# Kernel optimization log

Measured on AMD Instinct MI355X. Metric: run time of the kernel, lower is better.

The kernel has to match this reference:

```python
import jax, jax.numpy as jnp
import numpy as np

NUM_HEADS = 8
FOCUSING_FACTOR = 3
EPS = 1e-6


def _focus(x, f):
    # focusing: x**f, renormalized to keep the original L2 norm per token
    n = jnp.linalg.norm(x, axis=-1, keepdims=True)
    xp = x ** f
    return xp / jnp.linalg.norm(xp, axis=-1, keepdims=True) * n


def _split_heads(x, h):
    # b n (h c) -> (b h) n c
    b, n, C = x.shape
    return x.reshape(b, n, h, C // h).transpose(0, 2, 1, 3).reshape(b * h, n, C // h)


def setup_inputs() -> dict:
    key = jax.random.key(0)
    ks = jax.random.split(key, 9)
    B, Nq, Nkv, C = 8, 4096, 4096, 512
    query = jax.random.normal(ks[0], (B, Nq, C), jnp.float32)
    key_in = jax.random.normal(ks[1], (B, Nkv, C), jnp.float32)
    value = jax.random.normal(ks[2], (B, Nkv, C), jnp.float32)
    Wq = jax.random.normal(ks[3], (C, C), jnp.float32) * 0.02
    Wk = jax.random.normal(ks[4], (C, C), jnp.float32) * 0.02
    Wv = jax.random.normal(ks[5], (C, C), jnp.float32) * 0.02
    Wp = jax.random.normal(ks[6], (C, C), jnp.float32) * 0.02
    bp = jnp.zeros((C,), jnp.float32)
    scale = jax.random.normal(ks[7], (1, 1, C), jnp.float32) * 0.02
    return {"query": query, "key_in": key_in, "value": value,
            "Wq": Wq, "Wk": Wk, "Wv": Wv, "Wp": Wp, "bp": bp,
            "scale": scale, "H": 64, "W": 64}


def reference(query, key_in, value, Wq, Wk, Wv, Wp, bp, scale, H, W):
    B, N, C = query.shape
    h = NUM_HEADS
    # projections (qkv_bias=False)
    q = jax.nn.relu(query @ Wq) + EPS
    k = jax.nn.relu(key_in @ Wk) + EPS
    v = value @ Wv
    s = jax.nn.softplus(scale)  # [1,1,C]
    q = q / s
    k = k / s
    q = _focus(q, FOCUSING_FACTOR)
    k = _focus(k, FOCUSING_FACTOR)
    q = _split_heads(q, h)  # [(B h), N, c]
    k = _split_heads(k, h)
    v = _split_heads(v, h)
    # z-normalizer: 1 / (q . sum_j k_j)
    z = 1.0 / (jnp.einsum('bic,bc->bi', q, k.sum(axis=1)) + EPS)
    # O(n) kv-aggregation path (i*j*(c+d) > c*d*(i+j) for these shapes)
    kv = jnp.einsum('bjc,bjd->bcd', k, v)
    x = jnp.einsum('bic,bcd,bi->bid', q, kv, z)
    # (b h) n c -> b n (h c)
    x = x.reshape(B, h, N, C // h).transpose(0, 2, 1, 3).reshape(B, N, C)
    # note: dwc(v) feature_map in the original is dead code (never added to x)
    return x @ Wp + bp
```

## Files before the change

kernel.cpp:

```cpp
#include <hip/hip_runtime.h>
#include <hip/hip_bf16.h>
#include <math.h>

typedef __attribute__((ext_vector_type(8))) short short8;
typedef __attribute__((ext_vector_type(4))) float f32x4;

#define MFMA16x16x32(A,B,C) __builtin_amdgcn_mfma_f32_16x16x32_bf16((A),(B),(C),0,0,0)

__device__ __forceinline__ short f2b(float x) {
  __hip_bfloat16 h = __float2bfloat16(x);
  short s; __builtin_memcpy(&s, &h, 2); return s;
}
__device__ __forceinline__ float b2f(short s) {
  __hip_bfloat16 h; __builtin_memcpy(&h, &s, 2); return __bfloat162float(h);
}

__global__ __launch_bounds__(256)
void prep_kernel(const float* __restrict__ Wq, const float* __restrict__ Wk,
                 const float* __restrict__ Wv, const float* __restrict__ Wp,
                 const float* __restrict__ scale,
                 short* __restrict__ wpack, float* __restrict__ spls)
{
  const int b = blockIdx.x;
  const int t = threadIdx.x;
  if (b == 64) {
    for (int i = t; i < 512; i += 256) {
      float x = scale[i];
      spls[i] = (x > 20.f) ? x : log1pf(expf(x));
    }
    return;
  }
  const float* Ws[4] = {Wq, Wk, Wv, Wp};
  const int w = b >> 4, kf16 = b & 15;
  const float* W = Ws[w];
  short* dst = wpack + (size_t)w * (512 * 512);
  __shared__ short lds[32 * 512];
  for (int i = 0; i < 64; ++i) {
    int idx = i * 256 + t;
    int r = idx >> 9, c = idx & 511;
    lds[idx] = f2b(W[(size_t)(kf16 * 32 + r) * 512 + c]);
  }
  __syncthreads();
  for (int s = 0; s < 8; ++s) {
    int slot = s * 256 + t;
    int nf = slot >> 6, l = slot & 63;
    int n = nf * 16 + (l & 15);
    int k0 = 8 * (l >> 4);
    short8 v;
#pragma unroll
    for (int jj = 0; jj < 8; ++jj) v[jj] = lds[(k0 + jj) * 512 + n];
    *(short8*)(dst + ((size_t)(kf16 * 32 + nf) * 64 + l) * 8) = v;
  }
}

__global__ __launch_bounds__(512, 2)
void proj_kernel(const float* __restrict__ Aq, const float* __restrict__ Ak,
                 const float* __restrict__ Av, const short* __restrict__ Ax,
                 const short* __restrict__ wpack, const float* __restrict__ spls,
                 short* __restrict__ qf, short* __restrict__ kpk,
                 short* __restrict__ vpk, const float* __restrict__ bp,
                 float* __restrict__ outf, int mode_base)
{
  __shared__ char smem[65536];
  __shared__ float pnorm[2][8][64];
  __shared__ float facs[64];
  short* tile = (short*)smem;
  const int t = threadIdx.x;
  const int lane = t & 63;
  const int wid = t >> 6;
  const int g = lane >> 4;
  const int cl = lane & 15;
  const int bid = blockIdx.x;
  const int mode = (mode_base == 3) ? 3 : (bid >> 9);
  const int rb = (bid & 511) << 6;
  const int sr = t >> 3;
  const int sc = t & 7;
  const int r1 = bid & 3;
  const int r2 = (bid >> 2) & 3;

  const float* Af = (mode == 0) ? Aq : (mode == 1) ? Ak : Av;
  const short8* wp8 = (const short8*)(wpack + (size_t)mode * (512 * 512));

  {
    char* dst = smem + sr * 272 + sc * 32;
    if (mode < 3) {
      const float* src = Af + (size_t)(rb + sr) * 512 + r1 * 128 + sc * 16;
      f32x4 a0 = *(const f32x4*)(src);
      f32x4 a1 = *(const f32x4*)(src + 4);
      f32x4 a2 = *(const f32x4*)(src + 8);
      f32x4 a3 = *(const f32x4*)(src + 12);
      short8 v0, v1;
#pragma unroll
      for (int j = 0; j < 4; ++j) {
        v0[j] = f2b(a0[j]); v0[4 + j] = f2b(a1[j]);
        v1[j] = f2b(a2[j]); v1[4 + j] = f2b(a3[j]);
      }
      *(short8*)dst = v0; *(short8*)(dst + 16) = v1;
    } else {
      const short* src = Ax + (size_t)(rb + sr) * 512 + r1 * 128 + sc * 16;
      *(short8*)dst = *(const short8*)src;
      *(short8*)(dst + 16) = *(const short8*)(src + 8);
    }
  }
  f32x4 zero4 = {0.f, 0.f, 0.f, 0.f};
  f32x4 acc[4][4];
#pragma unroll
  for (int rf = 0; rf < 4; ++rf)
#pragma unroll
    for (int cf = 0; cf < 4; ++cf) acc[rf][cf] = zero4;

  short8 bcur[4], bnxt[4];
  {
    const int kf0 = r1 * 4 + r2;
#pragma unroll
    for (int cf = 0; cf < 4; ++cf)
      bcur[cf] = wp8[((size_t)(kf0 * 32 + wid * 4 + cf)) * 64 + lane];
  }
  __syncthreads();

#pragma unroll
  for (int sl = 0; sl < 4; ++sl) {
    const int s_phys = (sl + r1) & 3;
    const int s_next = (s_phys + 1) & 3;
    char* cur = smem + (sl & 1) * 17408;
    f32x4 rA0, rA1, rA2, rA3;
    short8 rB0, rB1;
    if (sl < 3) {
      if (mode < 3) {
        const float* src = Af + (size_t)(rb + sr) * 512 + s_next * 128 + sc * 16;
        rA0 = *(const f32x4*)(src);
        rA1 = *(const f32x4*)(src + 4);
        rA2 = *(const f32x4*)(src + 8);
        rA3 = *(const f32x4*)(src + 12);
      } else {
        const short* src = Ax + (size_t)(rb + sr) * 512 + s_next * 128 + sc * 16;
        rB0 = *(const short8*)src;
        rB1 = *(const short8*)(src + 8);
      }
    }
#pragma unroll
    for (int kl = 0; kl < 4; ++kl) {
      const int k_phys = (kl + r2) & 3;
      const bool last = (sl == 3) && (kl == 3);
      if (!last) {
        const int kf_n = (kl < 3) ? (s_phys * 4 + ((kl + 1 + r2) & 3))
                                  : (((s_phys + 1) & 3) * 4 + r2);
#pragma unroll
        for (int cf = 0; cf < 4; ++cf)
          bnxt[cf] = wp8[((size_t)(kf_n * 32 + wid * 4 + cf)) * 64 + lane];
      }
      short8 af[4];
#pragma unroll
      for (int rf = 0; rf < 4; ++rf)
        af[rf] = *(const short8*)(cur + (rf * 16 + cl) * 272 + k_phys * 64 + 16 * g);
#pragma unroll
      for (int rf = 0; rf < 4; ++rf)
#pragma unroll
        for (int cf = 0; cf < 4; ++cf)
          acc[rf][cf] = MFMA16x16x32(af[rf], bcur[cf], acc[rf][cf]);
      if (!last) {
#pragma unroll
        for (int cf = 0; cf < 4; ++cf) bcur[cf] = bnxt[cf];
      }
    }
    if (sl < 3) {
      char* dst = smem + ((sl + 1) & 1) * 17408 + sr * 272 + sc * 32;
      short8 v0, v1;
      if (mode < 3) {
#pragma unroll
        for (int j = 0; j < 4; ++j) {
          v0[j] = f2b(rA0[j]); v0[4 + j] = f2b(rA1[j]);
          v1[j] = f2b(rA2[j]); v1[4 + j] = f2b(rA3[j]);
        }
      } else { v0 = rB0; v1 = rB1; }
      *(short8*)dst = v0; *(short8*)(dst + 16) = v1;
      __syncthreads();
    }
  }

  if (mode == 3) {
#pragma unroll
    for (int rf = 0; rf < 4; ++rf)
#pragma unroll
      for (int cf = 0; cf < 4; ++cf) {
        int c = wid * 64 + cf * 16 + cl;
        float bv = bp[c];
#pragma unroll
        for (int j = 0; j < 4; ++j)
          outf[(size_t)(rb + rf * 16 + 4 * g + j) * 512 + c] = acc[rf][cf][j] + bv;
      }
    return;
  }

  if (mode < 2) {
    float sp_inv[4];
#pragma unroll
    for (int cf = 0; cf < 4; ++cf) sp_inv[cf] = 1.f / spls[wid * 64 + cf * 16 + cl];
    float p2[4][4], p6[4][4];
#pragma unroll
    for (int rf = 0; rf < 4; ++rf)
#pragma unroll
      for (int j = 0; j < 4; ++j) { p2[rf][j] = 0.f; p6[rf][j] = 0.f; }
#pragma unroll
    for (int rf = 0; rf < 4; ++rf)
#pragma unroll
      for (int cf = 0; cf < 4; ++cf)
#pragma unroll
        for (int j = 0; j < 4; ++j) {
          float v = acc[rf][cf][j];
          v = fmaxf(v, 0.f) + 1e-6f;
          v *= sp_inv[cf];
          acc[rf][cf][j] = v;
          float v2 = v * v;
          p2[rf][j] += v2;
          p6[rf][j] += v2 * v2 * v2;
        }
#pragma unroll
    for (int m = 1; m < 16; m <<= 1) {
#pragma unroll
      for (int rf = 0; rf < 4; ++rf)
#pragma unroll
        for (int j = 0; j < 4; ++j) {
          p2[rf][j] += __shfl_xor(p2[rf][j], m, 64);
          p6[rf][j] += __shfl_xor(p6[rf][j], m, 64);
        }
    }
    if (cl == 0) {
#pragma unroll
      for (int rf = 0; rf < 4; ++rf)
#pragma unroll
        for (int j = 0; j < 4; ++j) {
          pnorm[0][wid][rf * 16 + 4 * g + j] = p2[rf][j];
          pnorm[1][wid][rf * 16 + 4 * g + j] = p6[rf][j];
        }
    }
    __syncthreads();
    if (t < 64) {
      float a = 0.f, b = 0.f;
#pragma unroll
      for (int w = 0; w < 8; ++w) { a += pnorm[0][w][t]; b += pnorm[1][w][t]; }
      facs[t] = sqrtf(a / b);
    }
    __syncthreads();
    float fac[4][4];
#pragma unroll
    for (int rf = 0; rf < 4; ++rf)
#pragma unroll
      for (int j = 0; j < 4; ++j) fac[rf][j] = facs[rf * 16 + 4 * g + j];
#pragma unroll
    for (int rf = 0; rf < 4; ++rf)
#pragma unroll
      for (int cf = 0; cf < 4; ++cf)
#pragma unroll
        for (int j = 0; j < 4; ++j) {
          float v = acc[rf][cf][j];
          float o = v * v * v * fac[rf][j];
          int r = rf * 16 + 4 * g + j;
          int c = wid * 64 + cf * 16 + cl;
          int byteoff = (r * 1024 + c * 2) ^ ((r & 7) << 4);
          *(short*)((char*)tile + byteoff) = f2b(o);
        }
  } else {
    __syncthreads();
#pragma unroll
    for (int rf = 0; rf < 4; ++rf)
#pragma unroll
      for (int cf = 0; cf < 4; ++cf)
#pragma unroll
        for (int j = 0; j < 4; ++j) {
          int r = rf * 16 + 4 * g + j;
          int c = wid * 64 + cf * 16 + cl;
          int byteoff = (r * 1024 + c * 2) ^ ((r & 7) << 4);
          *(short*)((char*)tile + byteoff) = f2b(acc[rf][cf][j]);
        }
  }
  __syncthreads();

  if (mode == 0) {
    const int r = t >> 3;
    const int c8 = t & 7;
#pragma unroll
    for (int s = 0; s < 8; ++s) {
      int ci = c8 + 8 * s;
      int byteoff = (r * 1024 + ci * 16) ^ ((r & 7) << 4);
      short8 v = *(const short8*)((const char*)tile + byteoff);
      *(short8*)(qf + (size_t)(rb + r) * 512 + ci * 8) = v;
    }
  } else {
    short* dstp = (mode == 1) ? kpk : vpk;
    const int l = lane;
    const int batch = rb >> 12;
    const int jf_base = (rb & 4095) >> 5;
#pragma unroll
    for (int s = 0; s < 8; ++s) {
      int fidx = wid * 8 + s;
      int jf = fidx >> 5;
      int cf = fidx & 31;
      int c = cf * 16 + (l & 15);
      int j0 = jf * 32 + 8 * (l >> 4);
      short8 v;
#pragma unroll
      for (int jj = 0; jj < 8; ++jj) {
        int j = j0 + jj;
        int byteoff = (j * 1024 + c * 2) ^ ((j & 7) << 4);
        v[jj] = *(const short*)((const char*)tile + byteoff);
      }
      int bh = batch * 8 + (cf >> 2);
      int cfh = cf & 3;
      int jfg = jf_base + jf;
      *(short8*)(dstp + (((size_t)(bh * 128 + jfg) * 4 + cfh) * 64 + l) * 8) = v;
    }
  }
}

__global__ __launch_bounds__(256)
void kv_kernel(const short* __restrict__ kpack, const short* __restrict__ vpack,
               float* __restrict__ pKV, float* __restrict__ pKS)
{
  __shared__ float red[4][64 * 64];
  __shared__ float ksacc[64];
  const int t = threadIdx.x;
  const int lane = t & 63;
  const int w = t >> 6;
  const int g = lane >> 4;
  const int cl = lane & 15;
  const int bh = blockIdx.x >> 3;
  const int sp = blockIdx.x & 7;
  if (t < 64) ksacc[t] = 0.f;
  __syncthreads();

  f32x4 zero4 = {0.f, 0.f, 0.f, 0.f};
  f32x4 acc[4][4];
#pragma unroll
  for (int df = 0; df < 4; ++df)
#pragma unroll
    for (int cf = 0; cf < 4; ++cf) acc[df][cf] = zero4;
  float ks[4] = {0.f, 0.f, 0.f, 0.f};
  const short8* kp = (const short8*)kpack;
  const short8* vp = (const short8*)vpack;

#pragma unroll
  for (int i = 0; i < 4; ++i) {
    int jfg = sp * 16 + w * 4 + i;
    size_t base = ((size_t)bh * 128 + jfg) * 4 * 64;
    short8 afr[4], bfr[4];
#pragma unroll
    for (int f = 0; f < 4; ++f) {
      afr[f] = vp[base + (size_t)f * 64 + lane];
      bfr[f] = kp[base + (size_t)f * 64 + lane];
    }
#pragma unroll
    for (int cf = 0; cf < 4; ++cf) {
      float s = 0.f;
#pragma unroll
      for (int jj = 0; jj < 8; ++jj) s += b2f(bfr[cf][jj]);
      ks[cf] += s;
    }
#pragma unroll
    for (int df = 0; df < 4; ++df)
#pragma unroll
      for (int cf = 0; cf < 4; ++cf)
        acc[df][cf] = MFMA16x16x32(afr[df], bfr[cf], acc[df][cf]);
  }

#pragma unroll
  for (int cf = 0; cf < 4; ++cf) {
    ks[cf] += __shfl_xor(ks[cf], 16, 64);
    ks[cf] += __shfl_xor(ks[cf], 32, 64);
  }
  if (lane < 16) {
#pragma unroll
    for (int cf = 0; cf < 4; ++cf) atomicAdd(&ksacc[cf * 16 + lane], ks[cf]);
  }

#pragma unroll
  for (int df = 0; df < 4; ++df)
#pragma unroll
    for (int cf = 0; cf < 4; ++cf)
#pragma unroll
      for (int j = 0; j < 4; ++j)
        red[w][(df * 16 + 4 * g + j) * 64 + cf * 16 + cl] = acc[df][cf][j];
  __syncthreads();

  float* dkv = pKV + (size_t)blockIdx.x * 4096;
  for (int i = t; i < 4096; i += 256)
    dkv[i] = red[0][i] + red[1][i] + red[2][i] + red[3][i];
  if (t < 64) pKS[(size_t)blockIdx.x * 64 + t] = ksacc[t];
}

__global__ __launch_bounds__(256)
void kv_reduce(const float* __restrict__ pKV, const float* __restrict__ pKS,
               short* __restrict__ kvT, float* __restrict__ ksum)
{
  const int bh = blockIdx.x;
  const int t = threadIdx.x;
  for (int i = t; i < 4096; i += 256) {
    float s = 0.f;
#pragma unroll
    for (int sp = 0; sp < 8; ++sp) s += pKV[(size_t)(bh * 8 + sp) * 4096 + i];
    kvT[(size_t)bh * 4096 + i] = f2b(s);
  }
  if (t < 64) {
    float s = 0.f;
#pragma unroll
    for (int sp = 0; sp < 8; ++sp) s += pKS[(size_t)(bh * 8 + sp) * 64 + t];
    ksum[bh * 64 + t] = s;
  }
}

__global__ __launch_bounds__(512)
void x_kernel(const short* __restrict__ qf, const short* __restrict__ kvT,
              const float* __restrict__ ksum, short* __restrict__ xout)
{
  __shared__ short xt[64 * 512];
  __shared__ float ksb[512];
  __shared__ float zb[64 * 8];
  const int t = threadIdx.x;
  const int lane = t & 63;
  const int wid = t >> 6;
  const int wr = wid >> 1;
  const int wc = wid & 1;
  const int g = lane >> 4;
  const int cl = lane & 15;
  const int rb = blockIdx.x << 6;
  const int batch = rb >> 12;

  ksb[t] = ksum[batch * 512 + t];
  __syncthreads();

  {
    int r = t >> 3, h = t & 7;
    const short8* qrow = (const short8*)(qf + (size_t)(rb + r) * 512 + h * 64);
    float d = 0.f;
#pragma unroll
    for (int c8 = 0; c8 < 8; ++c8) {
      short8 qv = qrow[c8];
#pragma unroll
      for (int jj = 0; jj < 8; ++jj) d += b2f(qv[jj]) * ksb[h * 64 + c8 * 8 + jj];
    }
    zb[r * 8 + h] = 1.f / (d + 1e-6f);
  }
  __syncthreads();

  f32x4 zero4 = {0.f, 0.f, 0.f, 0.f};
  f32x4 xacc[16];
#pragma unroll
  for (int i = 0; i < 16; ++i) xacc[i] = zero4;

  const short8* q8 = (const short8*)qf;
  const size_t qrowbase = (size_t)(rb + wr * 16 + cl) * 64;
#pragma unroll
  for (int hh = 0; hh < 4; ++hh) {
    int h = wc * 4 + hh;
    short8 af0 = q8[qrowbase + h * 8 + g];
    short8 af1 = q8[qrowbase + h * 8 + 4 + g];
    const short8* kv8 = (const short8*)kvT + ((size_t)(batch * 8 + h)) * 512;
#pragma unroll
    for (int nfl = 0; nfl < 4; ++nfl) {
      short8 b0 = kv8[(size_t)(nfl * 16 + cl) * 8 + g];
      short8 b1 = kv8[(size_t)(nfl * 16 + cl) * 8 + 4 + g];
      int nf = hh * 4 + nfl;
      xacc[nf] = MFMA16x16x32(af0, b0, xacc[nf]);
      xacc[nf] = MFMA16x16x32(af1, b1, xacc[nf]);
    }
  }
#pragma unroll
  for (int hh = 0; hh < 4; ++hh) {
    int h = wc * 4 + hh;
    float z4[4];
#pragma unroll
    for (int j = 0; j < 4; ++j) z4[j] = zb[(wr * 16 + 4 * g + j) * 8 + h];
#pragma unroll
    for (int nfl = 0; nfl < 4; ++nfl) {
      int nf = hh * 4 + nfl;
#pragma unroll
      for (int j = 0; j < 4; ++j) {
        float xv = xacc[nf][j] * z4[j];
        int r = wr * 16 + 4 * g + j;
        int c = wc * 256 + nf * 16 + cl;
        int byteoff = (r * 1024 + c * 2) ^ ((r & 7) << 4);
        *(short*)((char*)xt + byteoff) = f2b(xv);
      }
    }
  }
  __syncthreads();

  const int r = t >> 3;
  const int c8 = t & 7;
#pragma unroll
  for (int s = 0; s < 8; ++s) {
    int ci = c8 + 8 * s;
    int byteoff = (r * 1024 + ci * 16) ^ ((r & 7) << 4);
    short8 v = *(const short8*)((const char*)xt + byteoff);
    *(short8*)(xout + (size_t)(rb + r) * 512 + ci * 8) = v;
  }
}

extern "C" void kernel_launch(void* const* d_in, const int* in_sizes, int n_in,
                              void* d_out, int out_size, void* d_ws, size_t ws_size,
                              hipStream_t stream)
{
  const float* query  = (const float*)d_in[0];
  const float* key_in = (const float*)d_in[1];
  const float* value  = (const float*)d_in[2];
  const float* Wq     = (const float*)d_in[3];
  const float* Wk     = (const float*)d_in[4];
  const float* Wv     = (const float*)d_in[5];
  const float* Wp     = (const float*)d_in[6];
  const float* bp     = (const float*)d_in[7];
  const float* scale  = (const float*)d_in[8];
  float* out = (float*)d_out;

  char* ws = (char*)d_ws;
  size_t off = 0;
  auto alloc = [&](size_t bytes) -> void* {
    void* p = ws + off;
    off += (bytes + 255) & ~(size_t)255;
    return p;
  };
  float* spls  = (float*)alloc(512 * 4);
  short* wpack = (short*)alloc((size_t)4 * 512 * 512 * 2);
  short* qf    = (short*)alloc((size_t)32768 * 512 * 2);
  short* kpack = (short*)alloc((size_t)32768 * 512 * 2);
  short* vpack = (short*)alloc((size_t)32768 * 512 * 2);
  float* pKV   = (float*)alloc((size_t)512 * 4096 * 4);
  float* pKS   = (float*)alloc((size_t)512 * 64 * 4);
  short* kvT   = (short*)alloc((size_t)64 * 4096 * 2);
  float* ksum  = (float*)alloc((size_t)64 * 64 * 4);
  short* xbuf  = kpack;

  prep_kernel<<<65, 256, 0, stream>>>(Wq, Wk, Wv, Wp, scale, wpack, spls);
  proj_kernel<<<1536, 512, 0, stream>>>(query, key_in, value, nullptr, wpack, spls,
                                        qf, kpack, vpack, nullptr, nullptr, 0);
  kv_kernel<<<512, 256, 0, stream>>>(kpack, vpack, pKV, pKS);
  kv_reduce<<<64, 256, 0, stream>>>(pKV, pKS, kvT, ksum);
  x_kernel<<<512, 512, 0, stream>>>(qf, kvT, ksum, xbuf);
  proj_kernel<<<512, 512, 0, stream>>>(nullptr, nullptr, nullptr, xbuf, wpack, spls,
                                       nullptr, nullptr, nullptr, bp, out, 3);
}
```

Measured before the change: 206.4 us.

## Retile QKV projection to 128x128 tiles with async LDS staging and split focus pass

The fused QKV projection moves from 64-row full-width tiles to 128x128 output tiles with a double-buffered k-loop. Weights are staged through global_load_lds, and setprio is raised around the MFMA block. Because a block no longer sees a full row, the per-row focus norms are accumulated with global atomics and the cube-and-rescale moves to a separate pass2 kernel that reads unfocused bf16 intermediates parked in the output buffer. This adds an extra read and write pass over Q and K plus a memset, in exchange for better operand reuse and more parallel blocks in the main GEMM.

Result: slower. 260.0 us (+26.0%).

```diff
diff --git a/kernel.cpp b/kernel.cpp
--- a/kernel.cpp
+++ b/kernel.cpp
@@ -3,9 +3,17 @@
 #include <math.h>
 
 typedef __attribute__((ext_vector_type(8))) short short8;
+typedef __attribute__((ext_vector_type(4))) short bf16x4;
 typedef __attribute__((ext_vector_type(4))) float f32x4;
 
 #define MFMA16x16x32(A,B,C) __builtin_amdgcn_mfma_f32_16x16x32_bf16((A),(B),(C),0,0,0)
+#define AS1(p) ((const __attribute__((address_space(1))) void*)(p))
+#define AS3(p) ((__attribute__((address_space(3))) void*)(p))
+#define WAITVM0() asm volatile("s_waitcnt vmcnt(0)" ::: "memory")
+#define WAITVM2() asm volatile("s_waitcnt vmcnt(2)" ::: "memory")
+#define WAITVM4() asm volatile("s_waitcnt vmcnt(4)" ::: "memory")
+#define LGKM0()   asm volatile("s_waitcnt lgkmcnt(0)" ::: "memory")
+#define BAR_LGKM() do { LGKM0(); __builtin_amdgcn_s_barrier(); } while (0)
 
 __device__ __forceinline__ short f2b(float x) {
   __hip_bfloat16 h = __float2bfloat16(x);
@@ -53,55 +61,67 @@
   }
 }
 
-__global__ __launch_bounds__(512, 2)
-void proj_kernel(const float* __restrict__ Aq, const float* __restrict__ Ak,
-                 const float* __restrict__ Av, const short* __restrict__ Ax,
-                 const short* __restrict__ wpack, const float* __restrict__ spls,
-                 short* __restrict__ qf, short* __restrict__ kpk,
-                 short* __restrict__ vpk, const float* __restrict__ bp,
-                 float* __restrict__ outf, int mode_base)
-{
-  __shared__ char smem[65536];
-  __shared__ float pnorm[2][8][64];
-  __shared__ float facs[64];
-  short* tile = (short*)smem;
+__global__ __launch_bounds__(256)
+void gemm128(const float* __restrict__ Aq, const float* __restrict__ Ak,
+             const float* __restrict__ Av, const short* __restrict__ wpack,
+             const float* __restrict__ spls,
+             short* __restrict__ yq, short* __restrict__ yk,
+             short* __restrict__ vpk,
+             float* __restrict__ gp2q, float* __restrict__ gp6q,
+             float* __restrict__ gp2k, float* __restrict__ gp6k)
+{
+  __shared__ __align__(128) char smem[32768];
+  __shared__ float pn2[2][128];
+  __shared__ float pn6[2][128];
   const int t = threadIdx.x;
   const int lane = t & 63;
   const int wid = t >> 6;
+  const int wr = wid >> 1;
+  const int wc = wid & 1;
   const int g = lane >> 4;
   const int cl = lane & 15;
   const int bid = blockIdx.x;
-  const int mode = (mode_base == 3) ? 3 : (bid >> 9);
-  const int rb = (bid & 511) << 6;
-  const int sr = t >> 3;
-  const int sc = t & 7;
-  const int r1 = bid & 3;
-  const int r2 = (bid >> 2) & 3;
+  const int mode = bid % 3;
+  const int rem = bid / 3;
+  const int cblk = rem & 3;
+  const int rblk = rem >> 2;
+  const int rb = rblk << 7;
+  const int cb = cblk << 7;
 
   const float* Af = (mode == 0) ? Aq : (mode == 1) ? Ak : Av;
-  const short8* wp8 = (const short8*)(wpack + (size_t)mode * (512 * 512));
-
-  {
-    char* dst = smem + sr * 272 + sc * 32;
-    if (mode < 3) {
-      const float* src = Af + (size_t)(rb + sr) * 512 + r1 * 128 + sc * 16;
-      f32x4 a0 = *(const f32x4*)(src);
-      f32x4 a1 = *(const f32x4*)(src + 4);
-      f32x4 a2 = *(const f32x4*)(src + 8);
-      f32x4 a3 = *(const f32x4*)(src + 12);
-      short8 v0, v1;
-#pragma unroll
-      for (int j = 0; j < 4; ++j) {
-        v0[j] = f2b(a0[j]); v0[4 + j] = f2b(a1[j]);
-        v1[j] = f2b(a2[j]); v1[4 + j] = f2b(a3[j]);
-      }
-      *(short8*)dst = v0; *(short8*)(dst + 16) = v1;
-    } else {
-      const short* src = Ax + (size_t)(rb + sr) * 512 + r1 * 128 + sc * 16;
-      *(short8*)dst = *(const short8*)src;
-      *(short8*)(dst + 16) = *(const short8*)(src + 8);
-    }
-  }
+  const char* wsrc = (const char*)(wpack + (size_t)mode * (512 * 512));
+  char* Ab0 = smem;
+  char* Ab1 = smem + 8192;
+  char* Bb0 = smem + 16384;
+  char* Bb1 = smem + 24576;
+
+  f32x4 ra[4];
+  auto loadA = [&](int kf) {
+#pragma unroll
+    for (int i = 0; i < 4; ++i) {
+      int chunk = i * 256 + t;
+      int row = chunk >> 3, sub = chunk & 7;
+      ra[i] = *(const f32x4*)(Af + (size_t)(rb + row) * 512 + kf * 32 + sub * 4);
+    }
+  };
+  auto writeA = [&](char* dst) {
+#pragma unroll
+    for (int i = 0; i < 4; ++i) {
+      int chunk = i * 256 + t;
+      int row = chunk >> 3, sub = chunk & 7;
+      bf16x4 v;
+      v[0] = f2b(ra[i][0]); v[1] = f2b(ra[i][1]);
+      v[2] = f2b(ra[i][2]); v[3] = f2b(ra[i][3]);
+      *(bf16x4*)(dst + (row >> 4) * 1024 + ((sub >> 1) * 16 + (row & 15)) * 16 + (sub & 1) * 8) = v;
+    }
+  };
+  auto stageB = [&](int kf, char* dst) {
+    const char* src = wsrc + ((size_t)(kf * 32 + cblk * 8)) * 1024;
+    const int off = t * 16;
+    __builtin_amdgcn_global_load_lds(AS1(src + off),        AS3(dst + off),        16, 0, 0);
+    __builtin_amdgcn_global_load_lds(AS1(src + 4096 + off), AS3(dst + 4096 + off), 16, 0, 0);
+  };
+
   f32x4 zero4 = {0.f, 0.f, 0.f, 0.f};
   f32x4 acc[4][4];
 #pragma unroll
@@ -109,93 +129,64 @@
 #pragma unroll
     for (int cf = 0; cf < 4; ++cf) acc[rf][cf] = zero4;
 
-  short8 bcur[4], bnxt[4];
+  loadA(0);
+  stageB(0, Bb0);
+  WAITVM2();
+  writeA(Ab0);
+  LGKM0();
+
+  for (int kf = 0; kf < 15; ++kf) {
+    char* Ac = (kf & 1) ? Ab1 : Ab0;
+    char* An = (kf & 1) ? Ab0 : Ab1;
+    char* Bc = (kf & 1) ? Bb1 : Bb0;
+    char* Bn = (kf & 1) ? Bb0 : Bb1;
+    loadA(kf + 1);
+    WAITVM4();
+    __builtin_amdgcn_s_barrier();
+    stageB(kf + 1, Bn);
+    short8 bfr[4], af[4];
+#pragma unroll
+    for (int cf = 0; cf < 4; ++cf)
+      bfr[cf] = *(const short8*)(Bc + ((wc * 4 + cf) * 64 + lane) * 16);
+#pragma unroll
+    for (int rf = 0; rf < 4; ++rf)
+      af[rf] = *(const short8*)(Ac + ((wr * 4 + rf) * 64 + lane) * 16);
+    __builtin_amdgcn_s_setprio(1);
+#pragma unroll
+    for (int rf = 0; rf < 4; ++rf)
+#pragma unroll
+      for (int cf = 0; cf < 4; ++cf)
+        acc[rf][cf] = MFMA16x16x32(af[rf], bfr[cf], acc[rf][cf]);
+    __builtin_amdgcn_s_setprio(0);
+    WAITVM2();
+    writeA(An);
+    LGKM0();
+  }
   {
-    const int kf0 = r1 * 4 + r2;
+    WAITVM0();
+    __builtin_amdgcn_s_barrier();
+    char* Ac = Ab1;
+    char* Bc = Bb1;
+    short8 bfr[4], af[4];
 #pragma unroll
     for (int cf = 0; cf < 4; ++cf)
-      bcur[cf] = wp8[((size_t)(kf0 * 32 + wid * 4 + cf)) * 64 + lane];
-  }
-  __syncthreads();
-
-#pragma unroll
-  for (int sl = 0; sl < 4; ++sl) {
-    const int s_phys = (sl + r1) & 3;
-    const int s_next = (s_phys + 1) & 3;
-    char* cur = smem + (sl & 1) * 17408;
-    f32x4 rA0, rA1, rA2, rA3;
-    short8 rB0, rB1;
-    if (sl < 3) {
-      if (mode < 3) {
-        const float* src = Af + (size_t)(rb + sr) * 512 + s_next * 128 + sc * 16;
-        rA0 = *(const f32x4*)(src);
-        rA1 = *(const f32x4*)(src + 4);
-        rA2 = *(const f32x4*)(src + 8);
-        rA3 = *(const f32x4*)(src + 12);
-      } else {
-        const short* src = Ax + (size_t)(rb + sr) * 512 + s_next * 128 + sc * 16;
-        rB0 = *(const short8*)src;
-        rB1 = *(const short8*)(src + 8);
-      }
-    }
-#pragma unroll
-    for (int kl = 0; kl < 4; ++kl) {
-      const int k_phys = (kl + r2) & 3;
-      const bool last = (sl == 3) && (kl == 3);
-      if (!last) {
-        const int kf_n = (kl < 3) ? (s_phys * 4 + ((kl + 1 + r2) & 3))
-                                  : (((s_phys + 1) & 3) * 4 + r2);
-#pragma unroll
-        for (int cf = 0; cf < 4; ++cf)
-          bnxt[cf] = wp8[((size_t)(kf_n * 32 + wid * 4 + cf)) * 64 + lane];
-      }
-      short8 af[4];
-#pragma unroll
-      for (int rf = 0; rf < 4; ++rf)
-        af[rf] = *(const short8*)(cur + (rf * 16 + cl) * 272 + k_phys * 64 + 16 * g);
-#pragma unroll
-      for (int rf = 0; rf < 4; ++rf)
-#pragma unroll
-        for (int cf = 0; cf < 4; ++cf)
-          acc[rf][cf] = MFMA16x16x32(af[rf], bcur[cf], acc[rf][cf]);
-      if (!last) {
-#pragma unroll
-        for (int cf = 0; cf < 4; ++cf) bcur[cf] = bnxt[cf];
-      }
-    }
-    if (sl < 3) {
-      char* dst = smem + ((sl + 1) & 1) * 17408 + sr * 272 + sc * 32;
-      short8 v0, v1;
-      if (mode < 3) {
-#pragma unroll
-        for (int j = 0; j < 4; ++j) {
-          v0[j] = f2b(rA0[j]); v0[4 + j] = f2b(rA1[j]);
-          v1[j] = f2b(rA2[j]); v1[4 + j] = f2b(rA3[j]);
-        }
-      } else { v0 = rB0; v1 = rB1; }
-      *(short8*)dst = v0; *(short8*)(dst + 16) = v1;
-      __syncthreads();
-    }
-  }
-
-  if (mode == 3) {
-#pragma unroll
-    for (int rf = 0; rf < 4; ++rf)
-#pragma unroll
-      for (int cf = 0; cf < 4; ++cf) {
-        int c = wid * 64 + cf * 16 + cl;
-        float bv = bp[c];
-#pragma unroll
-        for (int j = 0; j < 4; ++j)
-          outf[(size_t)(rb + rf * 16 + 4 * g + j) * 512 + c] = acc[rf][cf][j] + bv;
-      }
-    return;
-  }
+      bfr[cf] = *(const short8*)(Bc + ((wc * 4 + cf) * 64 + lane) * 16);
+#pragma unroll
+    for (int rf = 0; rf < 4; ++rf)
+      af[rf] = *(const short8*)(Ac + ((wr * 4 + rf) * 64 + lane) * 16);
+#pragma unroll
+    for (int rf = 0; rf < 4; ++rf)
+#pragma unroll
+      for (int cf = 0; cf < 4; ++cf)
+        acc[rf][cf] = MFMA16x16x32(af[rf], bfr[cf], acc[rf][cf]);
+  }
+  __syncthreads();
 
   if (mode < 2) {
     float sp_inv[4];
 #pragma unroll
-    for (int cf = 0; cf < 4; ++cf) sp_inv[cf] = 1.f / spls[wid * 64 + cf * 16 + cl];
+    for (int cf = 0; cf < 4; ++cf)
+      sp_inv[cf] = 1.f / spls[cb + wc * 64 + cf * 16 + cl];
     float p2[4][4], p6[4][4];
 #pragma unroll
     for (int rf = 0; rf < 4; ++rf)
@@ -230,70 +221,133 @@
       for (int rf = 0; rf < 4; ++rf)
 #pragma unroll
         for (int j = 0; j < 4; ++j) {
-          pnorm[0][wid][rf * 16 + 4 * g + j] = p2[rf][j];
-          pnorm[1][wid][rf * 16 + 4 * g + j] = p6[rf][j];
+          int r = wr * 64 + rf * 16 + 4 * g + j;
+          pn2[wc][r] = p2[rf][j];
+          pn6[wc][r] = p6[rf][j];
         }
     }
+#pragma unroll
+    for (int rf = 0; rf < 4; ++rf)
+#pragma unroll
+      for (int cf = 0; cf < 4; ++cf)
+#pragma unroll
+        for (int j = 0; j < 4; ++j) {
+          int r = wr * 64 + rf * 16 + 4 * g + j;
+          int c = wc * 64 + cf * 16 + cl;
+          int byteoff = (r * 256 + c * 2) ^ ((r & 7) << 4);
+          *(short*)(smem + byteoff) = f2b(acc[rf][cf][j]);
+        }
     __syncthreads();
-    if (t < 64) {
-      float a = 0.f, b = 0.f;
-#pragma unroll
-      for (int w = 0; w < 8; ++w) { a += pnorm[0][w][t]; b += pnorm[1][w][t]; }
-      facs[t] = sqrtf(a / b);
-    }
+    if (t < 128) {
+      float* g2 = (mode == 0) ? gp2q : gp2k;
+      float* g6 = (mode == 0) ? gp6q : gp6k;
+      atomicAdd(&g2[rb + t], pn2[0][t] + pn2[1][t]);
+      atomicAdd(&g6[rb + t], pn6[0][t] + pn6[1][t]);
+    }
+    short* ybuf = (mode == 0) ? yq : yk;
+#pragma unroll
+    for (int i = 0; i < 8; ++i) {
+      int chunk = i * 256 + t;
+      int row = chunk >> 4, c16 = chunk & 15;
+      int byteoff = (row * 256 + c16 * 16) ^ ((row & 7) << 4);
+      short8 v = *(const short8*)(smem + byteoff);
+      *(short8*)(ybuf + (size_t)(rb + row) * 512 + cb + c16 * 8) = v;
+    }
+  } else {
+#pragma unroll
+    for (int rf = 0; rf < 4; ++rf)
+#pragma unroll
+      for (int cf = 0; cf < 4; ++cf)
+#pragma unroll
+        for (int j = 0; j < 4; ++j) {
+          int r = wr * 64 + rf * 16 + 4 * g + j;
+          int c = wc * 64 + cf * 16 + cl;
+          int byteoff = (r * 256 + c * 2) ^ ((r & 7) << 4);
+          *(short*)(smem + byteoff) = f2b(acc[rf][cf][j]);
+        }
     __syncthreads();
-    float fac[4][4];
-#pragma unroll
-    for (int rf = 0; rf < 4; ++rf)
-#pragma unroll
-      for (int j = 0; j < 4; ++j) fac[rf][j] = facs[rf * 16 + 4 * g + j];
-#pragma unroll
-    for (int rf = 0; rf < 4; ++rf)
-#pragma unroll
-      for (int cf = 0; cf < 4; ++cf)
-#pragma unroll
-        for (int j = 0; j < 4; ++j) {
-          float v = acc[rf][cf][j];
-          float o = v * v * v * fac[rf][j];
-          int r = rf * 16 + 4 * g + j;
-          int c = wid * 64 + cf * 16 + cl;
-          int byteoff = (r * 1024 + c * 2) ^ ((r & 7) << 4);
-          *(short*)((char*)tile + byteoff) = f2b(o);
-        }
+    const int batch = rb >> 12;
+    const int jf_base = (rb & 4095) >> 5;
+    const int l = lane;
+#pragma unroll
+    for (int s = 0; s < 8; ++s) {
+      int fidx = wid * 8 + s;
+      int hl = fidx >> 4;
+      int cfh = (fidx >> 2) & 3;
+      int jf = fidx & 3;
+      int c = hl * 64 + cfh * 16 + (l & 15);
+      int j0 = jf * 32 + 8 * (l >> 4);
+      short8 v;
+#pragma unroll
+      for (int jj = 0; jj < 8; ++jj) {
+        int r = j0 + jj;
+        int byteoff = (r * 256 + c * 2) ^ ((r & 7) << 4);
+        v[jj] = *(const short*)(smem + byteoff);
+      }
+      int bh = batch * 8 + (cb >> 6) + hl;
+      int jfg = jf_base + jf;
+      *(short8*)(vpk + (((size_t)(bh * 128 + jfg) * 4 + cfh) * 64 + l) * 8) = v;
+    }
+  }
+}
+
+__global__ __launch_bounds__(256)
+void pass2(const short* __restrict__ yq, const short* __restrict__ yk,
+           const float* __restrict__ gp2q, const float* __restrict__ gp6q,
+           const float* __restrict__ gp2k, const float* __restrict__ gp6k,
+           short* __restrict__ qf, short* __restrict__ kpk)
+{
+  __shared__ char tile[65536];
+  __shared__ float facs[64];
+  const int t = threadIdx.x;
+  const int lane = t & 63;
+  const int wid = t >> 6;
+  const int bid = blockIdx.x;
+  const bool isk = bid >= 512;
+  const int rb = (bid & 511) << 6;
+  const short* ysrc = isk ? yk : yq;
+  const float* g2 = isk ? gp2k : gp2q;
+  const float* g6 = isk ? gp6k : gp6q;
+
+  if (t < 64) facs[t] = sqrtf(g2[rb + t] / g6[rb + t]);
+  __syncthreads();
+
+  if (!isk) {
+#pragma unroll
+    for (int i = 0; i < 16; ++i) {
+      int chunk = i * 256 + t;
+      int row = chunk >> 6, c8 = chunk & 63;
+      short8 v = *(const short8*)(ysrc + (size_t)(rb + row) * 512 + c8 * 8);
+      float fac = facs[row];
+#pragma unroll
+      for (int j = 0; j < 8; ++j) {
+        float y = b2f(v[j]);
+        v[j] = f2b(y * y * y * fac);
+      }
+      *(short8*)(qf + (size_t)(rb + row) * 512 + c8 * 8) = v;
+    }
   } else {
+#pragma unroll
+    for (int i = 0; i < 16; ++i) {
+      int chunk = i * 256 + t;
+      int row = chunk >> 6, c8 = chunk & 63;
+      short8 v = *(const short8*)(ysrc + (size_t)(rb + row) * 512 + c8 * 8);
+      float fac = facs[row];
+#pragma unroll
+      for (int j = 0; j < 8; ++j) {
+        float y = b2f(v[j]);
+        v[j] = f2b(y * y * y * fac);
+      }
+      int byteoff = (row * 1024 + c8 * 16) ^ ((row & 7) << 4);
+      *(short8*)(tile + byteoff) = v;
+    }
     __syncthreads();
-#pragma unroll
-    for (int rf = 0; rf < 4; ++rf)
-#pragma unroll
-      for (int cf = 0; cf < 4; ++cf)
-#pragma unroll
-        for (int j = 0; j < 4; ++j) {
-          int r = rf * 16 + 4 * g + j;
-          int c = wid * 64 + cf * 16 + cl;
-          int byteoff = (r * 1024 + c * 2) ^ ((r & 7) << 4);
-          *(short*)((char*)tile + byteoff) = f2b(acc[rf][cf][j]);
-        }
-  }
-  __syncthreads();
-
-  if (mode == 0) {
-    const int r = t >> 3;
-    const int c8 = t & 7;
-#pragma unroll
-    for (int s = 0; s < 8; ++s) {
-      int ci = c8 + 8 * s;
-      int byteoff = (r * 1024 + ci * 16) ^ ((r & 7) << 4);
-      short8 v = *(const short8*)((const char*)tile + byteoff);
-      *(short8*)(qf + (size_t)(rb + r) * 512 + ci * 8) = v;
-    }
-  } else {
-    short* dstp = (mode == 1) ? kpk : vpk;
     const int l = lane;
     const int batch = rb >> 12;
     const int jf_base = (rb & 4095) >> 5;
 #pragma unroll
-    for (int s = 0; s < 8; ++s) {
-      int fidx = wid * 8 + s;
+    for (int s = 0; s < 16; ++s) {
+      int fidx = wid * 16 + s;
       int jf = fidx >> 5;
       int cf = fidx & 31;
       int c = cf * 16 + (l & 15);
@@ -303,14 +357,113 @@
       for (int jj = 0; jj < 8; ++jj) {
         int j = j0 + jj;
         int byteoff = (j * 1024 + c * 2) ^ ((j & 7) << 4);
-        v[jj] = *(const short*)((const char*)tile + byteoff);
+        v[jj] = *(const short*)(tile + byteoff);
       }
       int bh = batch * 8 + (cf >> 2);
       int cfh = cf & 3;
       int jfg = jf_base + jf;
-      *(short8*)(dstp + (((size_t)(bh * 128 + jfg) * 4 + cfh) * 64 + l) * 8) = v;
-    }
-  }
+      *(short8*)(kpk + (((size_t)(bh * 128 + jfg) * 4 + cfh) * 64 + l) * 8) = v;
+    }
+  }
+}
+
+__global__ __launch_bounds__(512, 2)
+void proj_kernel(const short* __restrict__ Ax,
+                 const short* __restrict__ wpack,
+                 const float* __restrict__ bp, float* __restrict__ outf)
+{
+  __shared__ char smem[65536];
+  const int t = threadIdx.x;
+  const int lane = t & 63;
+  const int wid = t >> 6;
+  const int g = lane >> 4;
+  const int cl = lane & 15;
+  const int bid = blockIdx.x;
+  const int rb = bid << 6;
+  const int sr = t >> 3;
+  const int sc = t & 7;
+  const int r1 = bid & 3;
+  const int r2 = (bid >> 2) & 3;
+
+  const short8* wp8 = (const short8*)(wpack + (size_t)3 * (512 * 512));
+
+  {
+    char* dst = smem + sr * 272 + sc * 32;
+    const short* src = Ax + (size_t)(rb + sr) * 512 + r1 * 128 + sc * 16;
+    *(short8*)dst = *(const short8*)src;
+    *(short8*)(dst + 16) = *(const short8*)(src + 8);
+  }
+  f32x4 zero4 = {0.f, 0.f, 0.f, 0.f};
+  f32x4 acc[4][4];
+#pragma unroll
+  for (int rf = 0; rf < 4; ++rf)
+#pragma unroll
+    for (int cf = 0; cf < 4; ++cf) acc[rf][cf] = zero4;
+
+  short8 bcur[4], bnxt[4];
+  {
+    const int kf0 = r1 * 4 + r2;
+#pragma unroll
+    for (int cf = 0; cf < 4; ++cf)
+      bcur[cf] = wp8[((size_t)(kf0 * 32 + wid * 4 + cf)) * 64 + lane];
+  }
+  BAR_LGKM();
+
+#pragma unroll
+  for (int sl = 0; sl < 4; ++sl) {
+    const int s_phys = (sl + r1) & 3;
+    const int s_next = (s_phys + 1) & 3;
+    char* cur = smem + (sl & 1) * 17408;
+    short8 rB0, rB1;
+    if (sl < 3) {
+      const short* src = Ax + (size_t)(rb + sr) * 512 + s_next * 128 + sc * 16;
+      rB0 = *(const short8*)src;
+      rB1 = *(const short8*)(src + 8);
+    }
+#pragma unroll
+    for (int kl = 0; kl < 4; ++kl) {
+      const int k_phys = (kl + r2) & 3;
+      const bool last = (sl == 3) && (kl == 3);
+      if (!last) {
+        const int kf_n = (kl < 3) ? (s_phys * 4 + ((kl + 1 + r2) & 3))
+                                  : (((s_phys + 1) & 3) * 4 + r2);
+#pragma unroll
+        for (int cf = 0; cf < 4; ++cf)
+          bnxt[cf] = wp8[((size_t)(kf_n * 32 + wid * 4 + cf)) * 64 + lane];
+      }
+      short8 af[4];
+#pragma unroll
+      for (int rf = 0; rf < 4; ++rf)
+        af[rf] = *(const short8*)(cur + (rf * 16 + cl) * 272 + k_phys * 64 + 16 * g);
+      __builtin_amdgcn_s_setprio(1);
+#pragma unroll
+      for (int rf = 0; rf < 4; ++rf)
+#pragma unroll
+        for (int cf = 0; cf < 4; ++cf)
+          acc[rf][cf] = MFMA16x16x32(af[rf], bcur[cf], acc[rf][cf]);
+      __builtin_amdgcn_s_setprio(0);
+      if (!last) {
+#pragma unroll
+        for (int cf = 0; cf < 4; ++cf) bcur[cf] = bnxt[cf];
+      }
+    }
+    if (sl < 3) {
+      char* dst = smem + ((sl + 1) & 1) * 17408 + sr * 272 + sc * 32;
+      *(short8*)dst = rB0; *(short8*)(dst + 16) = rB1;
+      BAR_LGKM();
+    }
+  }
+
+#pragma unroll
+  for (int rf = 0; rf < 4; ++rf)
+#pragma unroll
+    for (int cf = 0; cf < 4; ++cf) {
+      int c = wid * 64 + cf * 16 + cl;
+      float bv = bp[c];
+#pragma unroll
+      for (int j = 0; j < 4; ++j)
+        outf[(size_t)(rb + rf * 16 + 4 * g + j) * 512 + c] = acc[rf][cf][j] + bv;
+    }
 }
 
 __global__ __launch_bounds__(256)
@@ -527,14 +680,19 @@
   float* pKS   = (float*)alloc((size_t)512 * 64 * 4);
   short* kvT   = (short*)alloc((size_t)64 * 4096 * 2);
   float* ksum  = (float*)alloc((size_t)64 * 64 * 4);
+  float* gp    = (float*)alloc((size_t)4 * 32768 * 4);
+  float* gp2q = gp, *gp6q = gp + 32768, *gp2k = gp + 65536, *gp6k = gp + 98304;
+  short* yq = (short*)d_out;
+  short* yk = yq + (size_t)32768 * 512;
   short* xbuf  = kpack;
 
   prep_kernel<<<65, 256, 0, stream>>>(Wq, Wk, Wv, Wp, scale, wpack, spls);
-  proj_kernel<<<1536, 512, 0, stream>>>(query, key_in, value, nullptr, wpack, spls,
-                                        qf, kpack, vpack, nullptr, nullptr, 0);
+  (void)hipMemsetAsync(gp, 0, (size_t)4 * 32768 * 4, stream);
+  gemm128<<<3072, 256, 0, stream>>>(query, key_in, value, wpack, spls,
+                                    yq, yk, vpack, gp2q, gp6q, gp2k, gp6k);
+  pass2<<<1024, 256, 0, stream>>>(yq, yk, gp2q, gp6q, gp2k, gp6k, qf, kpack);
   kv_kernel<<<512, 256, 0, stream>>>(kpack, vpack, pKV, pKS);
   kv_reduce<<<64, 256, 0, stream>>>(pKV, pKS, kvT, ksum);
   x_kernel<<<512, 512, 0, stream>>>(qf, kvT, ksum, xbuf);
-  proj_kernel<<<512, 512, 0, stream>>>(nullptr, nullptr, nullptr, xbuf, wpack, spls,
-                                       nullptr, nullptr, nullptr, bp, out, 3);
-}
+  proj_kernel<<<512, 512, 0, stream>>>(xbuf, wpack, bp, out);
+}
```
